# Optimization experiments

Hardware: AMD Instinct MI355X
Metric: run time of the kernel (lower is better)

Reference implementation:

```python
import jax, jax.numpy as jnp
import numpy as np

D_L, D_A, D_V = 300, 74, 35   # modality input dims
DH = 128                      # per-modality LSTM hidden
MEM = 256                     # memory dim
T, N = 512, 256               # time steps, batch
ATT_IN = 6 * DH               # 2 * total_h_dim (windowsize 2)


def _lin(x, W, b):
    return x @ W.T + b


def _lstm_cell(x, h, c, Wih, Whh, bih, bhh):
    g = x @ Wih.T + h @ Whh.T + bih + bhh
    i, f, gg, o = jnp.split(g, 4, axis=1)  # torch LSTMCell gate order
    c_new = jax.nn.sigmoid(f) * c + jax.nn.sigmoid(i) * jnp.tanh(gg)
    h_new = jax.nn.sigmoid(o) * jnp.tanh(c_new)
    return h_new, c_new


def setup_inputs() -> dict:
    key = jax.random.key(0)
    ks = iter(jax.random.split(key, 64))

    def w(shape):
        return jax.random.normal(next(ks), shape, jnp.float32) * 0.02

    inp = {
        "x": jax.random.normal(next(ks), (T, N, D_L + D_A + D_V), jnp.float32),
        "h_l_prior": w((N, DH)), "h_a_prior": w((N, DH)), "h_v_prior": w((N, DH)),
        "mem_prior": w((N, MEM)),
    }
    for m, din in (("l", D_L), ("a", D_A), ("v", D_V)):
        inp[f"Wih_{m}"] = w((4 * DH, din))
        inp[f"Whh_{m}"] = w((4 * DH, DH))
        inp[f"bih_{m}"] = w((4 * DH,))
        inp[f"bhh_{m}"] = w((4 * DH,))
    inp.update(
        att1_W1=w((256, ATT_IN)), att1_b1=w((256,)),
        att1_W2=w((ATT_IN, 256)), att1_b2=w((ATT_IN,)),
        att2_W1=w((256, ATT_IN)), att2_b1=w((256,)),
        att2_W2=w((MEM, 256)), att2_b2=w((MEM,)),
        g1_W1=w((256, ATT_IN + MEM)), g1_b1=w((256,)),
        g1_W2=w((MEM, 256)), g1_b2=w((MEM,)),
        g2_W1=w((256, ATT_IN + MEM)), g2_b1=w((256,)),
        g2_W2=w((MEM, 256)), g2_b2=w((MEM,)),
        out_W1=w((256, 3 * DH + MEM)), out_b1=w((256,)),
        out_W2=w((1, 256)), out_b2=w((1,)),
    )
    return inp


def reference(x, h_l_prior, h_a_prior, h_v_prior, mem_prior,
              Wih_l, Whh_l, bih_l, bhh_l,
              Wih_a, Whh_a, bih_a, bhh_a,
              Wih_v, Whh_v, bih_v, bhh_v,
              att1_W1, att1_b1, att1_W2, att1_b2,
              att2_W1, att2_b1, att2_W2, att2_b2,
              g1_W1, g1_b1, g1_W2, g1_b2,
              g2_W1, g2_b1, g2_W2, g2_b2,
              out_W1, out_b1, out_W2, out_b2):
    n = x.shape[1]
    # priors are accepted but zero-initialized inside the original forward
    z = lambda d: jnp.zeros((n, d), x.dtype)
    init = (z(DH), z(DH), z(DH), z(DH), z(DH), z(DH), z(MEM))

    def step(carry, xt):
        h_l, c_l, h_a, c_a, h_v, c_v, mem = carry
        x_l = xt[:, :D_L]
        x_a = xt[:, D_L:D_L + D_A]
        x_v = xt[:, D_L + D_A:]
        prev_cs = jnp.concatenate([c_l, c_a, c_v], axis=1)
        h_l, c_l = _lstm_cell(x_l, h_l, c_l, Wih_l, Whh_l, bih_l, bhh_l)
        h_a, c_a = _lstm_cell(x_a, h_a, c_a, Wih_a, Whh_a, bih_a, bhh_a)
        h_v, c_v = _lstm_cell(x_v, h_v, c_v, Wih_v, Whh_v, bih_v, bhh_v)
        new_cs = jnp.concatenate([c_l, c_a, c_v], axis=1)
        cStar = jnp.concatenate([prev_cs, new_cs], axis=1)  # [n, ATT_IN]
        attention = jax.nn.softmax(
            _lin(jax.nn.relu(_lin(cStar, att1_W1, att1_b1)), att1_W2, att1_b2), axis=1)
        attended = attention * cStar
        cHat = jnp.tanh(
            _lin(jax.nn.relu(_lin(attended, att2_W1, att2_b1)), att2_W2, att2_b2))
        both = jnp.concatenate([attended, mem], axis=1)  # [n, ATT_IN+MEM]
        gamma1 = jax.nn.sigmoid(
            _lin(jax.nn.relu(_lin(both, g1_W1, g1_b1)), g1_W2, g1_b2))
        gamma2 = jax.nn.sigmoid(
            _lin(jax.nn.relu(_lin(both, g2_W1, g2_b1)), g2_W2, g2_b2))
        mem = gamma1 * mem + gamma2 * cHat
        return (h_l, c_l, h_a, c_a, h_v, c_v, mem), None

    (h_l, c_l, h_a, c_a, h_v, c_v, mem), _ = jax.lax.scan(step, init, x)
    last_hs = jnp.concatenate([h_l, h_a, h_v, mem], axis=1)  # [n, 3*DH+MEM]
    return _lin(jax.nn.relu(_lin(last_hs, out_W1, out_b1)), out_W2, out_b2)
```

## Files before the change

### kernel.cpp

```cpp
#include <hip/hip_runtime.h>
#include <math.h>

#define TSTEPS 512
#define NBATCH 256
#define DLL 300
#define DAA 74
#define DVV 35
#define DX  409
#define DH  128
#define DMEM 256
#define CST 768

typedef unsigned short u16;
typedef unsigned int   u32;
typedef float v2f __attribute__((ext_vector_type(2)));
typedef _Float16 h2 __attribute__((ext_vector_type(2)));

__device__ __forceinline__ float sigf(float x){ return 1.0f/(1.0f+expf(-x)); }

__device__ __forceinline__ float d2(u32 w, u32 x, float c){
  return __builtin_amdgcn_fdot2(__builtin_bit_cast(h2,w), __builtin_bit_cast(h2,x), c, false);
}

__global__ void cast_pair(const float* __restrict__ src, _Float16* __restrict__ dst,
                          int OUT, int IN, int INP){
  int e = blockIdx.x*blockDim.x + threadIdx.x;
  if (e >= OUT*INP) return;
  int OUTH = OUT>>1;
  int j = e & 7;
  int s = (e>>3)&1;
  int q = e>>4;
  int cp = q % OUTH;
  int kb = q / OUTH;
  int k = kb*8 + j;
  int o = 2*cp + s;
  float v = (k < IN) ? src[o*IN + k] : 0.f;
  dst[e] = (_Float16)v;
}

struct P {
  const float* x;
  const float *bih_l,*bhh_l,*bih_a,*bhh_a,*bih_v,*bhh_v;
  const float *a1b1,*a1b2,*a2b1,*a2b2,*g1b1,*g1b2,*g2b1,*g2b2;
  const float *ob1,*ow2,*ob2;
  const _Float16 *ihl,*hhl,*iha,*hha,*ihv,*hhv;
  const _Float16 *a1w1,*a1w2,*a2w1,*a2w2,*g1w1,*g1w2,*g2w1,*g2w2,*ow1;
  float* out;
};

__device__ __forceinline__ void unitc(uint4 wa, uint4 wb, uint4 xa, uint4 xb,
    float&a00,float&a01,float&a10,float&a11){
  a00=d2(wa.x,xa.x,a00); a01=d2(wa.x,xb.x,a01); a10=d2(wb.x,xa.x,a10); a11=d2(wb.x,xb.x,a11);
  a00=d2(wa.y,xa.y,a00); a01=d2(wa.y,xb.y,a01); a10=d2(wb.y,xa.y,a10); a11=d2(wb.y,xb.y,a11);
  a00=d2(wa.z,xa.z,a00); a01=d2(wa.z,xb.z,a01); a10=d2(wb.z,xa.z,a10); a11=d2(wb.z,xb.z,a11);
  a00=d2(wa.w,xa.w,a00); a01=d2(wa.w,xb.w,a01); a10=d2(wb.w,xa.w,a10); a11=d2(wb.w,xb.w,a11);
}

template<int NKB, int OUTH>
__device__ __forceinline__ void sweep2(const uint4* __restrict__ wp,
    const _Float16* __restrict__ r0, const _Float16* __restrict__ r1,
    float&a00,float&a01,float&a10,float&a11){
  static_assert(NKB>=4 && (NKB&1)==0, "NKB even >=4");
  const int S = OUTH*2;
  uint4 p0a=wp[0], p0b=wp[1], p1a=wp[S], p1b=wp[S+1];
  const uint4* wn = wp + 2*S;
  int u=0;
  #pragma unroll 1
  for (; u+2<NKB; u+=2){
    uint4 n0a=wn[0], n0b=wn[1], n1a=wn[S], n1b=wn[S+1]; wn += 2*S;
    uint4 xa=*(const uint4*)(r0+u*8), xb=*(const uint4*)(r1+u*8);
    unitc(p0a,p0b,xa,xb,a00,a01,a10,a11);
    xa=*(const uint4*)(r0+u*8+8); xb=*(const uint4*)(r1+u*8+8);
    unitc(p1a,p1b,xa,xb,a00,a01,a10,a11);
    p0a=n0a; p0b=n0b; p1a=n1a; p1b=n1b;
  }
  {
    uint4 xa=*(const uint4*)(r0+u*8), xb=*(const uint4*)(r1+u*8);
    unitc(p0a,p0b,xa,xb,a00,a01,a10,a11);
    xa=*(const uint4*)(r0+u*8+8); xb=*(const uint4*)(r1+u*8+8);
    unitc(p1a,p1b,xa,xb,a00,a01,a10,a11);
  }
}

__device__ __forceinline__ int xfeat(int k){
  if (k < 300) return k;
  if (k < 320) return -1;
  if (k < 394) return k-20;
  if (k < 448) return -1;
  if (k < 483) return k-74;
  return -1;
}

__global__ void __launch_bounds__(512)
mfn_persistent(P p){
  __shared__ __align__(16) _Float16 s_x[1024];
  __shared__ __align__(16) _Float16 s_h[768];
  __shared__ __align__(16) _Float16 s_cs[1536];
  __shared__ __align__(16) _Float16 s_z[512];
  __shared__ __align__(16) _Float16 s_at[2048];
  __shared__ __align__(16) _Float16 s_z2[1536];
  __shared__ __align__(16) _Float16 s_last[1280];
  __shared__ __align__(16) float s_c2[768];
  __shared__ __align__(16) float s_csf[1536];
  __shared__ __align__(16) float s_mem[512];
  __shared__ __align__(16) float s_p[6144];
  __shared__ __align__(16) float s_bl[3][512];
  __shared__ __align__(16) float s_a1b1[256];
  __shared__ __align__(16) float s_a1b2[768];
  __shared__ __align__(16) float s_b6[6][256];
  __shared__ float s_red[16];

  const int tid = threadIdx.x;
  const int n0  = blockIdx.x*2;

  s_bl[0][tid]=p.bih_l[tid]+p.bhh_l[tid];
  s_bl[1][tid]=p.bih_a[tid]+p.bhh_a[tid];
  s_bl[2][tid]=p.bih_v[tid]+p.bhh_v[tid];
  s_mem[tid]=0.f;
  if (tid < 256){
    s_a1b1[tid]=p.a1b1[tid];
    s_b6[0][tid]=p.a2b1[tid]; s_b6[1][tid]=p.g1b1[tid]; s_b6[2][tid]=p.g2b1[tid];
    s_b6[3][tid]=p.a2b2[tid]; s_b6[4][tid]=p.g1b2[tid]; s_b6[5][tid]=p.g2b2[tid];
  }
  for (int i=tid;i<768;i+=512){ s_a1b2[i]=p.a1b2[i]; s_c2[i]=0.f; s_h[i]=(_Float16)0.f; }
  for (int i=tid;i<1024;i+=512){
    int r=i>>9, k=i&511, f=xfeat(k);
    float v = (f>=0)? p.x[(size_t)(n0+r)*DX + f] : 0.f;
    s_x[i]=(_Float16)v;
  }
  __syncthreads();

  for (int t=0; t<TSTEPS; t++){
    {
      const int cp=tid&255, kh=tid>>8;
      float a00,a01,a10,a11;
      a00=0.f;a01=0.f;a10=0.f;a11=0.f;
      sweep2<20,256>((const uint4*)p.ihl + kh*20*512 + cp*2, s_x+kh*160,     s_x+512+kh*160, a00,a01,a10,a11);
      sweep2< 8,256>((const uint4*)p.hhl + kh*8*512  + cp*2, s_h+kh*64,      s_h+128+kh*64,  a00,a01,a10,a11);
      *(v2f*)&s_p[        kh*1024 +       2*cp] = (v2f){a00,a10};
      *(v2f*)&s_p[        kh*1024 + 512 + 2*cp] = (v2f){a01,a11};
      a00=0.f;a01=0.f;a10=0.f;a11=0.f;
      sweep2< 8,256>((const uint4*)p.iha + kh*8*512 + cp*2, s_x+320+kh*64,  s_x+832+kh*64,  a00,a01,a10,a11);
      sweep2< 8,256>((const uint4*)p.hha + kh*8*512 + cp*2, s_h+256+kh*64,  s_h+384+kh*64,  a00,a01,a10,a11);
      *(v2f*)&s_p[2048 + kh*1024 +       2*cp] = (v2f){a00,a10};
      *(v2f*)&s_p[2048 + kh*1024 + 512 + 2*cp] = (v2f){a01,a11};
      a00=0.f;a01=0.f;a10=0.f;a11=0.f;
      sweep2< 4,256>((const uint4*)p.ihv + kh*4*512 + cp*2, s_x+448+kh*32,  s_x+960+kh*32,  a00,a01,a10,a11);
      sweep2< 8,256>((const uint4*)p.hhv + kh*8*512 + cp*2, s_h+512+kh*64,  s_h+640+kh*64,  a00,a01,a10,a11);
      *(v2f*)&s_p[4096 + kh*1024 +       2*cp] = (v2f){a00,a10};
      *(v2f*)&s_p[4096 + kh*1024 + 512 + 2*cp] = (v2f){a01,a11};
    }
    __syncthreads();

    for (int task=tid; task<768; task+=512){
      int m=task>>8, rem=task&255, u=rem>>1, r=rem&1;
      const float* pm = s_p + m*2048 + r*512;
      const float* bl = s_bl[m];
      float g0 = bl[u]     + pm[u]     + pm[1024+u];
      float g1 = bl[128+u] + pm[128+u] + pm[1024+128+u];
      float g2 = bl[256+u] + pm[256+u] + pm[1024+256+u];
      float g3 = bl[384+u] + pm[384+u] + pm[1024+384+u];
      float ig=sigf(g0), fg=sigf(g1), gg=tanhf(g2), og=sigf(g3);
      float co = s_c2[(m*2+r)*128+u];
      float c  = fg*co + ig*gg;
      float h  = og*tanhf(c);
      s_c2[(m*2+r)*128+u]=c;
      s_h[(m*2+r)*128+u]=(_Float16)h;
      s_csf[r*768 + m*128+u]     = co;  s_cs[r*768 + m*128+u]     = (_Float16)co;
      s_csf[r*768 + 384+m*128+u] = c;   s_cs[r*768 + 384+m*128+u] = (_Float16)c;
    }
    __syncthreads();

    if (tid < 256){
      int cp=tid&127, kh=tid>>7;
      float a00=0.f,a01=0.f,a10=0.f,a11=0.f;
      sweep2<48,128>((const uint4*)p.a1w1 + kh*48*256 + cp*2, s_cs+kh*384, s_cs+768+kh*384, a00,a01,a10,a11);
      *(v2f*)&s_p[kh*512 +       2*cp] = (v2f){a00,a10};
      *(v2f*)&s_p[kh*512 + 256 + 2*cp] = (v2f){a01,a11};
    } else if (t+1 < TSTEPS){
      const float* __restrict__ xb = p.x + (size_t)(t+1)*NBATCH*DX;
      for (int i2=tid-256; i2<1024; i2+=256){
        int r=i2>>9, k=i2&511, f=xfeat(k);
        if (f>=0) s_x[i2] = (_Float16)xb[(size_t)(n0+r)*DX + f];
      }
    }
    __syncthreads();

    {
      int c=tid&255, r=tid>>8;
      float z = s_a1b1[c] + s_p[r*256+c] + s_p[512+r*256+c];
      s_z[r*256+c] = (_Float16)fmaxf(z,0.f);
    }
    __syncthreads();

    if (tid < 384){
      float a00=0.f,a01=0.f,a10=0.f,a11=0.f;
      sweep2<32,384>((const uint4*)p.a1w2 + tid*2, s_z, s_z+256, a00,a01,a10,a11);
      *(v2f*)&s_p[      2*tid] = (v2f){a00,a10};
      *(v2f*)&s_p[768 + 2*tid] = (v2f){a01,a11};
    }
    __syncthreads();

    {
      int col=tid&255, rr=tid>>8;
      float s0 = s_a1b2[col]     + s_p[rr*768+col];
      float s1 = s_a1b2[256+col] + s_p[rr*768+256+col];
      float s2 = s_a1b2[512+col] + s_p[rr*768+512+col];
      float mx=fmaxf(fmaxf(s0,s1),s2);
      for (int off=32; off; off>>=1) mx=fmaxf(mx,__shfl_down(mx,off));
      if ((tid&63)==0) s_red[tid>>6]=mx;
      __syncthreads();
      float m = fmaxf(fmaxf(s_red[rr*4],s_red[rr*4+1]),fmaxf(s_red[rr*4+2],s_red[rr*4+3]));
      float e0=expf(s0-m), e1=expf(s1-m), e2=expf(s2-m);
      float ss=e0+e1+e2;
      for (int off=32; off; off>>=1) ss+=__shfl_down(ss,off);
      if ((tid&63)==0) s_red[8+(tid>>6)]=ss;
      s_at[rr*1024 + 768 + col] = (_Float16)s_mem[rr*256+col];
      __syncthreads();
      float inv=1.f/(s_red[8+rr*4]+s_red[8+rr*4+1]+s_red[8+rr*4+2]+s_red[8+rr*4+3]);
      s_at[rr*1024 + col]       = (_Float16)(e0*inv*s_csf[rr*768+col]);
      s_at[rr*1024 + 256 + col] = (_Float16)(e1*inv*s_csf[rr*768+256+col]);
      s_at[rr*1024 + 512 + col] = (_Float16)(e2*inv*s_csf[rr*768+512+col]);
    }
    __syncthreads();

    {
      int m4=tid>>7, cp=tid&127;
      if (m4==0){
        float a00=0.f,a01=0.f,a10=0.f,a11=0.f;
        sweep2<96,128>((const uint4*)p.a2w1 + cp*2, s_at, s_at+1024, a00,a01,a10,a11);
        *(v2f*)&s_p[      2*cp] = (v2f){a00,a10};
        *(v2f*)&s_p[256 + 2*cp] = (v2f){a01,a11};
      } else if (m4==1){
        float a00=0.f,a01=0.f,a10=0.f,a11=0.f;
        sweep2<128,128>((const uint4*)p.g1w1 + cp*2, s_at, s_at+1024, a00,a01,a10,a11);
        *(v2f*)&s_p[512 +       2*cp] = (v2f){a00,a10};
        *(v2f*)&s_p[512 + 256 + 2*cp] = (v2f){a01,a11};
      } else if (m4==2){
        float a00=0.f,a01=0.f,a10=0.f,a11=0.f;
        sweep2<128,128>((const uint4*)p.g2w1 + cp*2, s_at, s_at+1024, a00,a01,a10,a11);
        *(v2f*)&s_p[1024 +       2*cp] = (v2f){a00,a10};
        *(v2f*)&s_p[1024 + 256 + 2*cp] = (v2f){a01,a11};
      }
    }
    __syncthreads();

    for (int i=tid;i<1536;i+=512){
      int mu=i>>9, rem=i&511, r=rem>>8, c=rem&255;
      float v = s_b6[mu][c] + s_p[mu*512 + r*256 + c];
      s_z2[r*768 + mu*256 + c] = (_Float16)fmaxf(v,0.f);
    }
    __syncthreads();

    {
      int m4=tid>>7, cp=tid&127;
      if (m4<3){
        const _Float16* W = (m4==0)? p.a2w2 : ((m4==1)? p.g1w2 : p.g2w2);
        float a00=0.f,a01=0.f,a10=0.f,a11=0.f;
        sweep2<32,128>((const uint4*)W + cp*2, s_z2+m4*256, s_z2+768+m4*256, a00,a01,a10,a11);
        *(v2f*)&s_p[m4*512 +       2*cp] = (v2f){a00,a10};
        *(v2f*)&s_p[m4*512 + 256 + 2*cp] = (v2f){a01,a11};
      }
    }
    __syncthreads();

    {
      int c=tid&255, r=tid>>8;
      float ch  = s_b6[3][c] + s_p[r*256+c];
      float gm1 = s_b6[4][c] + s_p[512 + r*256+c];
      float gm2 = s_b6[5][c] + s_p[1024 + r*256+c];
      float mo = s_mem[r*256+c];
      s_mem[r*256+c] = sigf(gm1)*mo + sigf(gm2)*tanhf(ch);
    }
    __syncthreads();
  }

  for (int i=tid;i<1280;i+=512){
    int r=(i>=640)?1:0, j=i-r*640;
    _Float16 v = (j<384)? s_h[((j>>7)*2+r)*128 + (j&127)] : (_Float16)s_mem[r*256+(j-384)];
    s_last[r*640+j]=v;
  }
  __syncthreads();
  if (tid < 256){
    int cp=tid&127, kh=tid>>7;
    float a00=0.f,a01=0.f,a10=0.f,a11=0.f;
    sweep2<40,128>((const uint4*)p.ow1 + kh*40*256 + cp*2, s_last+kh*320, s_last+640+kh*320, a00,a01,a10,a11);
    *(v2f*)&s_p[kh*512 +       2*cp] = (v2f){a00,a10};
    *(v2f*)&s_p[kh*512 + 256 + 2*cp] = (v2f){a01,a11};
  }
  __syncthreads();
  {
    int c=tid&255, rr=tid>>8;
    float z = p.ob1[c] + s_p[rr*256+c] + s_p[512+rr*256+c];
    float pp = fmaxf(z,0.f)*p.ow2[c];
    for (int off=32; off; off>>=1) pp+=__shfl_down(pp,off);
    if ((tid&63)==0) s_red[tid>>6]=pp;
    __syncthreads();
    if (tid==0)   p.out[n0]   = s_red[0]+s_red[1]+s_red[2]+s_red[3]+p.ob2[0];
    if (tid==256) p.out[n0+1] = s_red[4]+s_red[5]+s_red[6]+s_red[7]+p.ob2[0];
  }
}

extern "C" void kernel_launch(void* const* d_in, const int* in_sizes, int n_in,
                              void* d_out, int out_size, void* d_ws, size_t ws_size,
                              hipStream_t stream){
  _Float16* ws = (_Float16*)d_ws;
  struct M { int src; size_t off; int OUT, IN, INP; };
  const M mats[15] = {
    { 5,       0, 512,  300, 320},
    { 6,  163840, 512,  128, 128},
    { 9,  229376, 512,   74, 128},
    {10,  294912, 512,  128, 128},
    {13,  360448, 512,   35,  64},
    {14,  393216, 512,  128, 128},
    {17,  458752, 256,  768, 768},
    {19,  655360, 768,  256, 256},
    {21,  851968, 256,  768, 768},
    {23, 1048576, 256,  256, 256},
    {25, 1114112, 256, 1024,1024},
    {27, 1376256, 256,  256, 256},
    {29, 1441792, 256, 1024,1024},
    {31, 1703936, 256,  256, 256},
    {33, 1769472, 256,  640, 640},
  };
  for (int i=0;i<15;i++){
    int total = mats[i].OUT*mats[i].INP;
    cast_pair<<<(total+255)/256, 256, 0, stream>>>(
        (const float*)d_in[mats[i].src], ws + mats[i].off,
        mats[i].OUT, mats[i].IN, mats[i].INP);
  }

  P p;
  p.x     = (const float*)d_in[0];
  p.bih_l = (const float*)d_in[7];  p.bhh_l = (const float*)d_in[8];
  p.bih_a = (const float*)d_in[11]; p.bhh_a = (const float*)d_in[12];
  p.bih_v = (const float*)d_in[15]; p.bhh_v = (const float*)d_in[16];
  p.a1b1  = (const float*)d_in[18]; p.a1b2  = (const float*)d_in[20];
  p.a2b1  = (const float*)d_in[22]; p.a2b2  = (const float*)d_in[24];
  p.g1b1  = (const float*)d_in[26]; p.g1b2  = (const float*)d_in[28];
  p.g2b1  = (const float*)d_in[30]; p.g2b2  = (const float*)d_in[32];
  p.ob1   = (const float*)d_in[34]; p.ow2   = (const float*)d_in[35];
  p.ob2   = (const float*)d_in[36];
  p.ihl   = ws + 0;       p.hhl  = ws + 163840;
  p.iha   = ws + 229376;  p.hha  = ws + 294912;
  p.ihv   = ws + 360448;  p.hhv  = ws + 393216;
  p.a1w1  = ws + 458752;  p.a1w2 = ws + 655360;
  p.a2w1  = ws + 851968;  p.a2w2 = ws + 1048576;
  p.g1w1  = ws + 1114112; p.g1w2 = ws + 1376256;
  p.g2w1  = ws + 1441792; p.g2w2 = ws + 1703936;
  p.ow1   = ws + 1769472;
  p.out   = (float*)d_out;

  mfn_persistent<<<NBATCH/2, 512, 0, stream>>>(p);
}
```

Before: 17.14 ms.

## Double block size to 1024 threads with split-K partial sums per matvec

Launches 1024 threads per block instead of 512 and splits the K dimension of every per-step matvec (LSTM gates, attention, gamma MLPs) over more thread groups. Partial sums go to a doubled shared buffer and are added in the following elementwise stages. The goal is a shorter serial dot-product chain per thread in the latency-bound recurrent loop, since only 128 blocks run on a large GPU. The costs are more shared memory, more partial-sum reads, larger register pressure limits under the 1024 launch bound, and some idle threads in several phases.

```diff
diff --git a/kernel.cpp b/kernel.cpp
--- a/kernel.cpp
+++ b/kernel.cpp
@@ -91,7 +91,7 @@
   return -1;
 }
 
-__global__ void __launch_bounds__(512)
+__global__ void __launch_bounds__(1024)
 mfn_persistent(P p){
   __shared__ __align__(16) _Float16 s_x[1024];
   __shared__ __align__(16) _Float16 s_h[768];
@@ -103,7 +103,7 @@
   __shared__ __align__(16) float s_c2[768];
   __shared__ __align__(16) float s_csf[1536];
   __shared__ __align__(16) float s_mem[512];
-  __shared__ __align__(16) float s_p[6144];
+  __shared__ __align__(16) float s_p[12288];
   __shared__ __align__(16) float s_bl[3][512];
   __shared__ __align__(16) float s_a1b1[256];
   __shared__ __align__(16) float s_a1b2[768];
@@ -113,20 +113,22 @@
   const int tid = threadIdx.x;
   const int n0  = blockIdx.x*2;
 
-  s_bl[0][tid]=p.bih_l[tid]+p.bhh_l[tid];
-  s_bl[1][tid]=p.bih_a[tid]+p.bhh_a[tid];
-  s_bl[2][tid]=p.bih_v[tid]+p.bhh_v[tid];
-  s_mem[tid]=0.f;
+  if (tid < 512){
+    s_bl[0][tid]=p.bih_l[tid]+p.bhh_l[tid];
+    s_bl[1][tid]=p.bih_a[tid]+p.bhh_a[tid];
+    s_bl[2][tid]=p.bih_v[tid]+p.bhh_v[tid];
+    s_mem[tid]=0.f;
+  }
   if (tid < 256){
     s_a1b1[tid]=p.a1b1[tid];
     s_b6[0][tid]=p.a2b1[tid]; s_b6[1][tid]=p.g1b1[tid]; s_b6[2][tid]=p.g2b1[tid];
     s_b6[3][tid]=p.a2b2[tid]; s_b6[4][tid]=p.g1b2[tid]; s_b6[5][tid]=p.g2b2[tid];
   }
-  for (int i=tid;i<768;i+=512){ s_a1b2[i]=p.a1b2[i]; s_c2[i]=0.f; s_h[i]=(_Float16)0.f; }
-  for (int i=tid;i<1024;i+=512){
-    int r=i>>9, k=i&511, f=xfeat(k);
+  if (tid < 768){ s_a1b2[tid]=p.a1b2[tid]; s_c2[tid]=0.f; s_h[tid]=(_Float16)0.f; }
+  {
+    int r=tid>>9, k=tid&511, f=xfeat(k);
     float v = (f>=0)? p.x[(size_t)(n0+r)*DX + f] : 0.f;
-    s_x[i]=(_Float16)v;
+    s_x[tid]=(_Float16)v;
   }
   __syncthreads();
 
@@ -135,31 +137,32 @@
       const int cp=tid&255, kh=tid>>8;
       float a00,a01,a10,a11;
       a00=0.f;a01=0.f;a10=0.f;a11=0.f;
-      sweep2<20,256>((const uint4*)p.ihl + kh*20*512 + cp*2, s_x+kh*160,     s_x+512+kh*160, a00,a01,a10,a11);
-      sweep2< 8,256>((const uint4*)p.hhl + kh*8*512  + cp*2, s_h+kh*64,      s_h+128+kh*64,  a00,a01,a10,a11);
+      sweep2<10,256>((const uint4*)p.ihl + kh*10*512 + cp*2, s_x+kh*80,      s_x+512+kh*80,  a00,a01,a10,a11);
+      sweep2< 4,256>((const uint4*)p.hhl + kh*4*512  + cp*2, s_h+kh*32,      s_h+128+kh*32,  a00,a01,a10,a11);
       *(v2f*)&s_p[        kh*1024 +       2*cp] = (v2f){a00,a10};
       *(v2f*)&s_p[        kh*1024 + 512 + 2*cp] = (v2f){a01,a11};
       a00=0.f;a01=0.f;a10=0.f;a11=0.f;
-      sweep2< 8,256>((const uint4*)p.iha + kh*8*512 + cp*2, s_x+320+kh*64,  s_x+832+kh*64,  a00,a01,a10,a11);
-      sweep2< 8,256>((const uint4*)p.hha + kh*8*512 + cp*2, s_h+256+kh*64,  s_h+384+kh*64,  a00,a01,a10,a11);
-      *(v2f*)&s_p[2048 + kh*1024 +       2*cp] = (v2f){a00,a10};
-      *(v2f*)&s_p[2048 + kh*1024 + 512 + 2*cp] = (v2f){a01,a11};
-      a00=0.f;a01=0.f;a10=0.f;a11=0.f;
-      sweep2< 4,256>((const uint4*)p.ihv + kh*4*512 + cp*2, s_x+448+kh*32,  s_x+960+kh*32,  a00,a01,a10,a11);
-      sweep2< 8,256>((const uint4*)p.hhv + kh*8*512 + cp*2, s_h+512+kh*64,  s_h+640+kh*64,  a00,a01,a10,a11);
+      sweep2< 4,256>((const uint4*)p.iha + kh*4*512 + cp*2, s_x+320+kh*32,  s_x+832+kh*32,  a00,a01,a10,a11);
+      sweep2< 4,256>((const uint4*)p.hha + kh*4*512 + cp*2, s_h+256+kh*32,  s_h+384+kh*32,  a00,a01,a10,a11);
       *(v2f*)&s_p[4096 + kh*1024 +       2*cp] = (v2f){a00,a10};
       *(v2f*)&s_p[4096 + kh*1024 + 512 + 2*cp] = (v2f){a01,a11};
-    }
-    __syncthreads();
-
-    for (int task=tid; task<768; task+=512){
-      int m=task>>8, rem=task&255, u=rem>>1, r=rem&1;
-      const float* pm = s_p + m*2048 + r*512;
+      a00=0.f;a01=0.f;a10=0.f;a11=0.f;
+      if (kh < 2)
+        sweep2<4,256>((const uint4*)p.ihv + kh*4*512 + cp*2, s_x+448+kh*32, s_x+960+kh*32, a00,a01,a10,a11);
+      sweep2< 4,256>((const uint4*)p.hhv + kh*4*512 + cp*2, s_h+512+kh*32,  s_h+640+kh*32,  a00,a01,a10,a11);
+      *(v2f*)&s_p[8192 + kh*1024 +       2*cp] = (v2f){a00,a10};
+      *(v2f*)&s_p[8192 + kh*1024 + 512 + 2*cp] = (v2f){a01,a11};
+    }
+    __syncthreads();
+
+    if (tid < 768){
+      int m=tid>>8, rem=tid&255, u=rem>>1, r=rem&1;
+      const float* pm = s_p + m*4096 + r*512;
       const float* bl = s_bl[m];
-      float g0 = bl[u]     + pm[u]     + pm[1024+u];
-      float g1 = bl[128+u] + pm[128+u] + pm[1024+128+u];
-      float g2 = bl[256+u] + pm[256+u] + pm[1024+256+u];
-      float g3 = bl[384+u] + pm[384+u] + pm[1024+384+u];
+      float g0 = bl[u]     + pm[u]     + pm[1024+u]     + pm[2048+u]     + pm[3072+u];
+      float g1 = bl[128+u] + pm[128+u] + pm[1024+128+u] + pm[2048+128+u] + pm[3072+128+u];
+      float g2 = bl[256+u] + pm[256+u] + pm[1024+256+u] + pm[2048+256+u] + pm[3072+256+u];
+      float g3 = bl[384+u] + pm[384+u] + pm[1024+384+u] + pm[2048+384+u] + pm[3072+384+u];
       float ig=sigf(g0), fg=sigf(g1), gg=tanhf(g2), og=sigf(g3);
       float co = s_c2[(m*2+r)*128+u];
       float c  = fg*co + ig*gg;
@@ -171,114 +174,129 @@
     }
     __syncthreads();
 
-    if (tid < 256){
+    if (tid < 512){
       int cp=tid&127, kh=tid>>7;
       float a00=0.f,a01=0.f,a10=0.f,a11=0.f;
-      sweep2<48,128>((const uint4*)p.a1w1 + kh*48*256 + cp*2, s_cs+kh*384, s_cs+768+kh*384, a00,a01,a10,a11);
+      sweep2<24,128>((const uint4*)p.a1w1 + kh*24*256 + cp*2, s_cs+kh*192, s_cs+768+kh*192, a00,a01,a10,a11);
       *(v2f*)&s_p[kh*512 +       2*cp] = (v2f){a00,a10};
       *(v2f*)&s_p[kh*512 + 256 + 2*cp] = (v2f){a01,a11};
     } else if (t+1 < TSTEPS){
       const float* __restrict__ xb = p.x + (size_t)(t+1)*NBATCH*DX;
-      for (int i2=tid-256; i2<1024; i2+=256){
+      #pragma unroll
+      for (int q=0;q<2;q++){
+        int i2 = (tid-512) + q*512;
         int r=i2>>9, k=i2&511, f=xfeat(k);
         if (f>=0) s_x[i2] = (_Float16)xb[(size_t)(n0+r)*DX + f];
       }
     }
     __syncthreads();
 
+    if (tid < 512){
+      int c=tid&255, r=tid>>8;
+      float z = s_a1b1[c] + s_p[r*256+c] + s_p[512+r*256+c] + s_p[1024+r*256+c] + s_p[1536+r*256+c];
+      s_z[r*256+c] = (_Float16)fmaxf(z,0.f);
+    }
+    __syncthreads();
+
+    if (tid < 768){
+      int kh = (tid>=384)?1:0;
+      int cp = tid - 384*kh;
+      float a00=0.f,a01=0.f,a10=0.f,a11=0.f;
+      sweep2<16,384>((const uint4*)p.a1w2 + kh*16*768 + cp*2, s_z+kh*128, s_z+256+kh*128, a00,a01,a10,a11);
+      *(v2f*)&s_p[kh*1536 +       2*cp] = (v2f){a00,a10};
+      *(v2f*)&s_p[kh*1536 + 768 + 2*cp] = (v2f){a01,a11};
+    }
+    __syncthreads();
+
     {
-      int c=tid&255, r=tid>>8;
-      float z = s_a1b1[c] + s_p[r*256+c] + s_p[512+r*256+c];
-      s_z[r*256+c] = (_Float16)fmaxf(z,0.f);
-    }
-    __syncthreads();
-
-    if (tid < 384){
-      float a00=0.f,a01=0.f,a10=0.f,a11=0.f;
-      sweep2<32,384>((const uint4*)p.a1w2 + tid*2, s_z, s_z+256, a00,a01,a10,a11);
-      *(v2f*)&s_p[      2*tid] = (v2f){a00,a10};
-      *(v2f*)&s_p[768 + 2*tid] = (v2f){a01,a11};
-    }
-    __syncthreads();
-
-    {
-      int col=tid&255, rr=tid>>8;
-      float s0 = s_a1b2[col]     + s_p[rr*768+col];
-      float s1 = s_a1b2[256+col] + s_p[rr*768+256+col];
-      float s2 = s_a1b2[512+col] + s_p[rr*768+512+col];
-      float mx=fmaxf(fmaxf(s0,s1),s2);
-      for (int off=32; off; off>>=1) mx=fmaxf(mx,__shfl_down(mx,off));
-      if ((tid&63)==0) s_red[tid>>6]=mx;
+      int col=tid&255, rr=(tid>>8)&1;
+      float s0=0.f,s1=0.f,s2=0.f;
+      if (tid < 512){
+        s0 = s_a1b2[col]     + s_p[rr*768+col]     + s_p[1536+rr*768+col];
+        s1 = s_a1b2[256+col] + s_p[rr*768+256+col] + s_p[1536+rr*768+256+col];
+        s2 = s_a1b2[512+col] + s_p[rr*768+512+col] + s_p[1536+rr*768+512+col];
+        float mx=fmaxf(fmaxf(s0,s1),s2);
+        for (int off=32; off; off>>=1) mx=fmaxf(mx,__shfl_down(mx,off));
+        if ((tid&63)==0) s_red[tid>>6]=mx;
+      }
       __syncthreads();
-      float m = fmaxf(fmaxf(s_red[rr*4],s_red[rr*4+1]),fmaxf(s_red[rr*4+2],s_red[rr*4+3]));
-      float e0=expf(s0-m), e1=expf(s1-m), e2=expf(s2-m);
-      float ss=e0+e1+e2;
-      for (int off=32; off; off>>=1) ss+=__shfl_down(ss,off);
-      if ((tid&63)==0) s_red[8+(tid>>6)]=ss;
-      s_at[rr*1024 + 768 + col] = (_Float16)s_mem[rr*256+col];
+      float e0=0.f,e1=0.f,e2=0.f;
+      if (tid < 512){
+        float m = fmaxf(fmaxf(s_red[rr*4],s_red[rr*4+1]),fmaxf(s_red[rr*4+2],s_red[rr*4+3]));
+        e0=expf(s0-m); e1=expf(s1-m); e2=expf(s2-m);
+        float ss=e0+e1+e2;
+        for (int off=32; off; off>>=1) ss+=__shfl_down(ss,off);
+        if ((tid&63)==0) s_red[8+(tid>>6)]=ss;
+        s_at[rr*1024 + 768 + col] = (_Float16)s_mem[rr*256+col];
+      }
       __syncthreads();
-      float inv=1.f/(s_red[8+rr*4]+s_red[8+rr*4+1]+s_red[8+rr*4+2]+s_red[8+rr*4+3]);
-      s_at[rr*1024 + col]       = (_Float16)(e0*inv*s_csf[rr*768+col]);
-      s_at[rr*1024 + 256 + col] = (_Float16)(e1*inv*s_csf[rr*768+256+col]);
-      s_at[rr*1024 + 512 + col] = (_Float16)(e2*inv*s_csf[rr*768+512+col]);
-    }
-    __syncthreads();
-
-    {
-      int m4=tid>>7, cp=tid&127;
+      if (tid < 512){
+        float inv=1.f/(s_red[8+rr*4]+s_red[8+rr*4+1]+s_red[8+rr*4+2]+s_red[8+rr*4+3]);
+        s_at[rr*1024 + col]       = (_Float16)(e0*inv*s_csf[rr*768+col]);
+        s_at[rr*1024 + 256 + col] = (_Float16)(e1*inv*s_csf[rr*768+256+col]);
+        s_at[rr*1024 + 512 + col] = (_Float16)(e2*inv*s_csf[rr*768+512+col]);
+      }
+    }
+    __syncthreads();
+
+    if (tid < 768){
+      int m4=tid>>8, cp=tid&127, kh=(tid>>7)&1;
       if (m4==0){
         float a00=0.f,a01=0.f,a10=0.f,a11=0.f;
-        sweep2<96,128>((const uint4*)p.a2w1 + cp*2, s_at, s_at+1024, a00,a01,a10,a11);
-        *(v2f*)&s_p[      2*cp] = (v2f){a00,a10};
-        *(v2f*)&s_p[256 + 2*cp] = (v2f){a01,a11};
+        sweep2<48,128>((const uint4*)p.a2w1 + kh*48*256 + cp*2, s_at+kh*384, s_at+1024+kh*384, a00,a01,a10,a11);
+        *(v2f*)&s_p[kh*512 +       2*cp] = (v2f){a00,a10};
+        *(v2f*)&s_p[kh*512 + 256 + 2*cp] = (v2f){a01,a11};
       } else if (m4==1){
         float a00=0.f,a01=0.f,a10=0.f,a11=0.f;
-        sweep2<128,128>((const uint4*)p.g1w1 + cp*2, s_at, s_at+1024, a00,a01,a10,a11);
-        *(v2f*)&s_p[512 +       2*cp] = (v2f){a00,a10};
-        *(v2f*)&s_p[512 + 256 + 2*cp] = (v2f){a01,a11};
-      } else if (m4==2){
+        sweep2<64,128>((const uint4*)p.g1w1 + kh*64*256 + cp*2, s_at+kh*512, s_at+1024+kh*512, a00,a01,a10,a11);
+        *(v2f*)&s_p[1024 + kh*512 +       2*cp] = (v2f){a00,a10};
+        *(v2f*)&s_p[1024 + kh*512 + 256 + 2*cp] = (v2f){a01,a11};
+      } else {
         float a00=0.f,a01=0.f,a10=0.f,a11=0.f;
-        sweep2<128,128>((const uint4*)p.g2w1 + cp*2, s_at, s_at+1024, a00,a01,a10,a11);
-        *(v2f*)&s_p[1024 +       2*cp] = (v2f){a00,a10};
-        *(v2f*)&s_p[1024 + 256 + 2*cp] = (v2f){a01,a11};
-      }
-    }
-    __syncthreads();
-
-    for (int i=tid;i<1536;i+=512){
-      int mu=i>>9, rem=i&511, r=rem>>8, c=rem&255;
-      float v = s_b6[mu][c] + s_p[mu*512 + r*256 + c];
-      s_z2[r*768 + mu*256 + c] = (_Float16)fmaxf(v,0.f);
-    }
-    __syncthreads();
-
-    {
-      int m4=tid>>7, cp=tid&127;
-      if (m4<3){
-        const _Float16* W = (m4==0)? p.a2w2 : ((m4==1)? p.g1w2 : p.g2w2);
-        float a00=0.f,a01=0.f,a10=0.f,a11=0.f;
-        sweep2<32,128>((const uint4*)W + cp*2, s_z2+m4*256, s_z2+768+m4*256, a00,a01,a10,a11);
-        *(v2f*)&s_p[m4*512 +       2*cp] = (v2f){a00,a10};
-        *(v2f*)&s_p[m4*512 + 256 + 2*cp] = (v2f){a01,a11};
-      }
-    }
-    __syncthreads();
-
-    {
+        sweep2<64,128>((const uint4*)p.g2w1 + kh*64*256 + cp*2, s_at+kh*512, s_at+1024+kh*512, a00,a01,a10,a11);
+        *(v2f*)&s_p[2048 + kh*512 +       2*cp] = (v2f){a00,a10};
+        *(v2f*)&s_p[2048 + kh*512 + 256 + 2*cp] = (v2f){a01,a11};
+      }
+    }
+    __syncthreads();
+
+    if (tid < 1024){
+      for (int i=tid;i<1536;i+=1024){
+        int mu=i>>9, rem=i&511, r=rem>>8, c=rem&255;
+        float v = s_b6[mu][c] + s_p[mu*1024 + r*256 + c] + s_p[mu*1024 + 512 + r*256 + c];
+        s_z2[r*768 + mu*256 + c] = (_Float16)fmaxf(v,0.f);
+      }
+    }
+    __syncthreads();
+
+    if (tid < 768){
+      int m4=tid>>8, cp=tid&127, kh=(tid>>7)&1;
+      const _Float16* W = (m4==0)? p.a2w2 : ((m4==1)? p.g1w2 : p.g2w2);
+      float a00=0.f,a01=0.f,a10=0.f,a11=0.f;
+      sweep2<16,128>((const uint4*)W + kh*16*256 + cp*2,
+                     s_z2+m4*256+kh*128, s_z2+768+m4*256+kh*128, a00,a01,a10,a11);
+      *(v2f*)&s_p[m4*1024 + kh*512 +       2*cp] = (v2f){a00,a10};
+      *(v2f*)&s_p[m4*1024 + kh*512 + 256 + 2*cp] = (v2f){a01,a11};
+    }
+    __syncthreads();
+
+    if (tid < 512){
       int c=tid&255, r=tid>>8;
-      float ch  = s_b6[3][c] + s_p[r*256+c];
-      float gm1 = s_b6[4][c] + s_p[512 + r*256+c];
-      float gm2 = s_b6[5][c] + s_p[1024 + r*256+c];
+      float ch  = s_b6[3][c] + s_p[r*256+c]      + s_p[512+r*256+c];
+      float gm1 = s_b6[4][c] + s_p[1024+r*256+c] + s_p[1024+512+r*256+c];
+      float gm2 = s_b6[5][c] + s_p[2048+r*256+c] + s_p[2048+512+r*256+c];
       float mo = s_mem[r*256+c];
       s_mem[r*256+c] = sigf(gm1)*mo + sigf(gm2)*tanhf(ch);
     }
     __syncthreads();
   }
 
-  for (int i=tid;i<1280;i+=512){
-    int r=(i>=640)?1:0, j=i-r*640;
-    _Float16 v = (j<384)? s_h[((j>>7)*2+r)*128 + (j&127)] : (_Float16)s_mem[r*256+(j-384)];
-    s_last[r*640+j]=v;
+  if (tid < 1024){
+    for (int i=tid;i<1280;i+=1024){
+      int r=(i>=640)?1:0, j=i-r*640;
+      _Float16 v = (j<384)? s_h[((j>>7)*2+r)*128 + (j&127)] : (_Float16)s_mem[r*256+(j-384)];
+      s_last[r*640+j]=v;
+    }
   }
   __syncthreads();
   if (tid < 256){
@@ -290,11 +308,14 @@
   }
   __syncthreads();
   {
-    int c=tid&255, rr=tid>>8;
-    float z = p.ob1[c] + s_p[rr*256+c] + s_p[512+rr*256+c];
-    float pp = fmaxf(z,0.f)*p.ow2[c];
-    for (int off=32; off; off>>=1) pp+=__shfl_down(pp,off);
-    if ((tid&63)==0) s_red[tid>>6]=pp;
+    int c=tid&255, rr=(tid>>8)&1;
+    float pp = 0.f;
+    if (tid < 512){
+      float z = p.ob1[c] + s_p[rr*256+c] + s_p[512+rr*256+c];
+      pp = fmaxf(z,0.f)*p.ow2[c];
+      for (int off=32; off; off>>=1) pp+=__shfl_down(pp,off);
+      if ((tid&63)==0) s_red[tid>>6]=pp;
+    }
     __syncthreads();
     if (tid==0)   p.out[n0]   = s_red[0]+s_red[1]+s_red[2]+s_red[3]+p.ob2[0];
     if (tid==256) p.out[n0+1] = s_red[4]+s_red[5]+s_red[6]+s_red[7]+p.ob2[0];
@@ -351,5 +372,5 @@
   p.ow1   = ws + 1769472;
   p.out   = (float*)d_out;
 
-  mfn_persistent<<<NBATCH/2, 512, 0, stream>>>(p);
-}
+  mfn_persistent<<<NBATCH/2, 1024, 0, stream>>>(p);
+}
```

Measured after the change: 20.37 ms. +18.8%, slower.

## Split-K the attention and gate GEMVs across all warps and relocate x prefetch

Applied to the files above, without the earlier changes.

The first attention layer now splits its K dimension four ways so all 512 threads compute it, where before only 256 did. The second-stage attention and gate layers are rebalanced with split-K so every thread does equal work instead of one idle group of 128. The prefetch of the next timestep's x moves into the idle threads of the a1w2 phase. The partial sums are combined in the following bias and ReLU phase, which adds shared-memory reads and needs a larger s_p scratch region (up to 4096 floats).

```diff
diff --git a/kernel.cpp b/kernel.cpp
--- a/kernel.cpp
+++ b/kernel.cpp
@@ -171,24 +171,19 @@
     }
     __syncthreads();
 
-    if (tid < 256){
+    {
       int cp=tid&127, kh=tid>>7;
       float a00=0.f,a01=0.f,a10=0.f,a11=0.f;
-      sweep2<48,128>((const uint4*)p.a1w1 + kh*48*256 + cp*2, s_cs+kh*384, s_cs+768+kh*384, a00,a01,a10,a11);
+      sweep2<24,128>((const uint4*)p.a1w1 + kh*24*256 + cp*2, s_cs+kh*192, s_cs+768+kh*192, a00,a01,a10,a11);
       *(v2f*)&s_p[kh*512 +       2*cp] = (v2f){a00,a10};
       *(v2f*)&s_p[kh*512 + 256 + 2*cp] = (v2f){a01,a11};
-    } else if (t+1 < TSTEPS){
-      const float* __restrict__ xb = p.x + (size_t)(t+1)*NBATCH*DX;
-      for (int i2=tid-256; i2<1024; i2+=256){
-        int r=i2>>9, k=i2&511, f=xfeat(k);
-        if (f>=0) s_x[i2] = (_Float16)xb[(size_t)(n0+r)*DX + f];
-      }
     }
     __syncthreads();
 
     {
       int c=tid&255, r=tid>>8;
-      float z = s_a1b1[c] + s_p[r*256+c] + s_p[512+r*256+c];
+      float z = s_a1b1[c] + s_p[r*256+c] + s_p[512+r*256+c]
+                          + s_p[1024+r*256+c] + s_p[1536+r*256+c];
       s_z[r*256+c] = (_Float16)fmaxf(z,0.f);
     }
     __syncthreads();
@@ -198,6 +193,14 @@
       sweep2<32,384>((const uint4*)p.a1w2 + tid*2, s_z, s_z+256, a00,a01,a10,a11);
       *(v2f*)&s_p[      2*tid] = (v2f){a00,a10};
       *(v2f*)&s_p[768 + 2*tid] = (v2f){a01,a11};
+    } else if (t+1 < TSTEPS){
+      const float* __restrict__ xb = p.x + (size_t)(t+1)*NBATCH*DX;
+      #pragma unroll
+      for (int q=0;q<8;q++){
+        int i2 = (tid-384) + q*128;
+        int r=i2>>9, k=i2&511, f=xfeat(k);
+        if (f>=0) s_x[i2] = (_Float16)xb[(size_t)(n0+r)*DX + f];
+      }
     }
     __syncthreads();
 
@@ -225,29 +228,30 @@
     __syncthreads();
 
     {
-      int m4=tid>>7, cp=tid&127;
-      if (m4==0){
-        float a00=0.f,a01=0.f,a10=0.f,a11=0.f;
-        sweep2<96,128>((const uint4*)p.a2w1 + cp*2, s_at, s_at+1024, a00,a01,a10,a11);
-        *(v2f*)&s_p[      2*cp] = (v2f){a00,a10};
-        *(v2f*)&s_p[256 + 2*cp] = (v2f){a01,a11};
-      } else if (m4==1){
-        float a00=0.f,a01=0.f,a10=0.f,a11=0.f;
-        sweep2<128,128>((const uint4*)p.g1w1 + cp*2, s_at, s_at+1024, a00,a01,a10,a11);
-        *(v2f*)&s_p[512 +       2*cp] = (v2f){a00,a10};
-        *(v2f*)&s_p[512 + 256 + 2*cp] = (v2f){a01,a11};
-      } else if (m4==2){
-        float a00=0.f,a01=0.f,a10=0.f,a11=0.f;
-        sweep2<128,128>((const uint4*)p.g2w1 + cp*2, s_at, s_at+1024, a00,a01,a10,a11);
-        *(v2f*)&s_p[1024 +       2*cp] = (v2f){a00,a10};
-        *(v2f*)&s_p[1024 + 256 + 2*cp] = (v2f){a01,a11};
-      }
+      int cp=tid&127, kh4=tid>>7;
+      float a00=0.f,a01=0.f,a10=0.f,a11=0.f;
+      sweep2<24,128>((const uint4*)p.a2w1 + kh4*24*256 + cp*2, s_at+kh4*192, s_at+1024+kh4*192, a00,a01,a10,a11);
+      *(v2f*)&s_p[kh4*512 +       2*cp] = (v2f){a00,a10};
+      *(v2f*)&s_p[kh4*512 + 256 + 2*cp] = (v2f){a01,a11};
+      int mg = tid>>8, kh = (tid>>7)&1;
+      const _Float16* W = mg ? p.g2w1 : p.g1w1;
+      a00=0.f;a01=0.f;a10=0.f;a11=0.f;
+      sweep2<64,128>((const uint4*)W + kh*64*256 + cp*2, s_at+kh*512, s_at+1024+kh*512, a00,a01,a10,a11);
+      *(v2f*)&s_p[2048 + mg*1024 + kh*512 +       2*cp] = (v2f){a00,a10};
+      *(v2f*)&s_p[2048 + mg*1024 + kh*512 + 256 + 2*cp] = (v2f){a01,a11};
     }
     __syncthreads();
 
     for (int i=tid;i<1536;i+=512){
       int mu=i>>9, rem=i&511, r=rem>>8, c=rem&255;
-      float v = s_b6[mu][c] + s_p[mu*512 + r*256 + c];
+      float v;
+      if (mu==0)
+        v = s_b6[0][c] + s_p[r*256+c] + s_p[512+r*256+c]
+                       + s_p[1024+r*256+c] + s_p[1536+r*256+c];
+      else {
+        const float* q = s_p + 2048 + (mu-1)*1024;
+        v = s_b6[mu][c] + q[r*256+c] + q[512+r*256+c];
+      }
       s_z2[r*768 + mu*256 + c] = (_Float16)fmaxf(v,0.f);
     }
     __syncthreads();
```

Measured after the change: 15.34 ms (median of 2 runs). 10.5% less time.
